# Kernel tuning notes

Measured on AMD Instinct MI355X. Metric: run time of the kernel, lower is better.

The kernel has to match this reference:

```python
import jax, jax.numpy as jnp
import numpy as np

N_WINDOWS = 4
WIN_H, WIN_W = 512, 512          # module 'size'
IMG_H, IMG_W = 1024, 1024        # 2x2 tiling of windows
N_MASKS = 32                     # n_windows * masks_per_window
MPW = N_MASKS // N_WINDOWS       # 8 masks per window (channel 0 of each block = background)
SLOT_DIM = 64
SIM_THRESH = 0.1                 # module 'similarity'


def setup_inputs() -> dict:
    key = jax.random.key(0)
    k1, k2 = jax.random.split(key)
    masks = jax.random.normal(k1, (1, N_MASKS, IMG_H, IMG_W), dtype=jnp.float32)
    slot_features = jax.random.normal(k2, (N_WINDOWS, MPW - 1, SLOT_DIM), dtype=jnp.float32)
    # static window layout, equivalent to keys ['w_0_0','w_512_0','w_0_512','w_512_512']
    pad_left = jnp.array([0, WIN_W, 0, WIN_W], dtype=jnp.int32)
    pad_top = jnp.array([0, 0, WIN_H, WIN_H], dtype=jnp.int32)
    return {"masks": masks, "slot_features": slot_features,
            "pad_left": pad_left, "pad_top": pad_top}


def _merge_windows(masks, slot_features, pl, pt):
    """pl, pt: python int lists (static metadata parsed from keys)."""
    B, C, H, W = masks.shape
    mpw = C // N_WINDOWS

    # --- to_one_hot: argmax over channel dim, one-hot back to [B,C,H,W] float ---
    ids = jnp.argmax(masks, axis=1)                                   # [B,H,W]
    m = jnp.moveaxis(jax.nn.one_hot(ids, C, dtype=masks.dtype), -1, 1)  # [B,C,H,W]

    ranges = [(i * mpw, (i + 1) * mpw) for i in range(N_WINDOWS)]

    # --- adjacency over window pads (static) ---
    adjacency = []
    for i in range(N_WINDOWS):
        for j in range(i + 1, N_WINDOWS):
            if pt[i] == pt[j] and abs(pl[i] - pl[j]) == WIN_W:
                adjacency.append((i, j, True) if pl[i] < pl[j] else (j, i, True))
            if pl[i] == pl[j] and abs(pt[i] - pt[j]) == WIN_H:
                adjacency.append((i, j, False) if pt[i] < pt[j] else (j, i, False))

    # --- per-channel edge-touch booleans (vectorized replacement of set building) ---
    edge_l = jnp.zeros((C,), bool)
    edge_r = jnp.zeros((C,), bool)
    edge_t = jnp.zeros((C,), bool)
    edge_b = jnp.zeros((C,), bool)
    for wi, (s, e) in enumerate(ranges):
        ys, ye = max(pt[wi], 0), min(pt[wi] + WIN_H, H)
        xs, xe = max(pl[wi], 0), min(pl[wi] + WIN_W, W)
        if ys >= ye or xs >= xe:
            continue
        win = m[0, s:e, ys:ye, xs:xe]                # [mpw, hh, ww]
        edge_l = edge_l.at[s:e].set(jnp.any(win[:, :, 0] == 1, axis=-1))
        edge_r = edge_r.at[s:e].set(jnp.any(win[:, :, -1] == 1, axis=-1))
        edge_t = edge_t.at[s:e].set(jnp.any(win[:, 0, :] == 1, axis=-1))
        edge_b = edge_b.at[s:e].set(jnp.any(win[:, -1, :] == 1, axis=-1))

    # --- static candidate pair list (background channels ci % mpw == 0 excluded) ---
    ci_l, cj_l, wi_l, wj_l, hz_l = [], [], [], [], []
    for wi, wj, horiz in adjacency:
        si, ei = ranges[wi]
        sj, ej = ranges[wj]
        for ci in range(si + 1, ei):
            for cj in range(sj + 1, ej):
                ci_l.append(ci); cj_l.append(cj)
                wi_l.append(wi); wj_l.append(wj); hz_l.append(horiz)
    P = len(ci_l)
    if P == 0:
        return m

    ci_a = jnp.array(ci_l, jnp.int32)
    cj_a = jnp.array(cj_l, jnp.int32)
    horiz = jnp.array(hz_l)

    # --- cosine similarities for all pairs at once ---
    sf_n = slot_features / (jnp.linalg.norm(slot_features, axis=-1, keepdims=True) + 1e-8)
    rel_i = np.array(ci_l) % mpw - 1
    rel_j = np.array(cj_l) % mpw - 1
    fi = sf_n[np.array(wi_l), rel_i]                 # [P, D]
    fj = sf_n[np.array(wj_l), rel_j]
    sims = jnp.sum(fi * fj, axis=-1)                 # [P]

    edge_ok = jnp.where(horiz, edge_r[ci_a] & edge_l[cj_a], edge_b[ci_a] & edge_t[cj_a])
    passing = edge_ok & (sims > SIM_THRESH)          # [P]

    # --- sequential dedup/merge scan (order-dependent, like the torch loop) ---
    def step(carry, xs):
        m, merged = carry
        ci, cj, ok = xs
        cond = ok & ~merged[ci] & ~merged[cj]
        keep = jnp.minimum(ci, cj)
        rem = jnp.maximum(ci, cj)
        rem_ch = jnp.take(m, rem, axis=1)            # [B,H,W]
        m = m.at[:, keep].add(jnp.where(cond, rem_ch, 0.0))
        m = m.at[:, rem].set(jnp.where(cond, jnp.zeros_like(rem_ch), rem_ch))
        merged = merged.at[rem].set(merged[rem] | cond)
        return (m, merged), None

    (m, _), _ = jax.lax.scan(step, (m, jnp.zeros((C,), bool)), (ci_a, cj_a, passing))
    return m


def reference(masks, slot_features, pad_left, pad_top):
    # pads encode the (static) window layout parsed from the string keys
    pl = [int(v) for v in np.asarray(pad_left)]
    pt = [int(v) for v in np.asarray(pad_top)]
    return _merge_windows(masks, slot_features, pl, pt)
```

## Files before the change

### kernel.cpp

```cpp
#include <hip/hip_runtime.h>

#define IMG_H 1024
#define IMG_W 1024
#define NPIX (IMG_H * IMG_W)
#define N_MASKS 32
#define N_WINDOWS 4
#define MPW 8
#define WIN_H 512
#define WIN_W 512
#define SIM_THRESH 0.1f
#define NBLK 1024

typedef float vf4 __attribute__((ext_vector_type(4)));

#define WS_EDGE  0
#define WS_IDS   (NBLK * 16)

__global__ __launch_bounds__(256) void k_argmax(const float* __restrict__ masks,
                                                const int* __restrict__ pl,
                                                const int* __restrict__ pt,
                                                uint4* __restrict__ edge_blocks,
                                                unsigned char* __restrict__ ids) {
    __shared__ int spl[4], spt[4];
    __shared__ unsigned sem[4];
    const int tid = threadIdx.x;
    if (tid < 4) { spl[tid] = pl[tid]; spt[tid] = pt[tid]; sem[tid] = 0u; }
    __syncthreads();

    const int idx = (blockIdx.x * 256 + tid) * 4;

    float bv0, bv1, bv2, bv3;
    int bc0 = 0, bc1 = 0, bc2 = 0, bc3 = 0;
    {
        const float4 v = *(const float4*)(masks + idx);
        bv0 = v.x; bv1 = v.y; bv2 = v.z; bv3 = v.w;
    }
#pragma unroll
    for (int c = 1; c < N_MASKS; c++) {
        const float4 v = *(const float4*)(masks + (size_t)c * NPIX + idx);
        if (v.x > bv0) { bv0 = v.x; bc0 = c; }
        if (v.y > bv1) { bv1 = v.y; bc1 = c; }
        if (v.z > bv2) { bv2 = v.z; bc2 = c; }
        if (v.w > bv3) { bv3 = v.w; bc3 = c; }
    }
    *(uchar4*)(ids + idx) = make_uchar4((unsigned char)bc0, (unsigned char)bc1,
                                        (unsigned char)bc2, (unsigned char)bc3);

    const int y = idx >> 10;
    const int x0 = idx & (IMG_W - 1);
    const int bcs[4] = {bc0, bc1, bc2, bc3};
#pragma unroll
    for (int wi = 0; wi < N_WINDOWS; wi++) {
        const int xs = max(spl[wi], 0), xe = min(spl[wi] + WIN_W, IMG_W);
        const int ys = max(spt[wi], 0), ye = min(spt[wi] + WIN_H, IMG_H);
        if (ys >= ye || xs >= xe) continue;
        if (y < ys || y >= ye) continue;
#pragma unroll
        for (int k = 0; k < 4; k++) {
            const int x = x0 + k;
            if (x < xs || x >= xe) continue;
            const int c = bcs[k];
            if ((c >> 3) != wi) continue;
            const unsigned bit = 1u << c;
            if (x == xs)     atomicOr(&sem[0], bit);
            if (x == xe - 1) atomicOr(&sem[1], bit);
            if (y == ys)     atomicOr(&sem[2], bit);
            if (y == ye - 1) atomicOr(&sem[3], bit);
        }
    }
    __syncthreads();
    if (tid == 0) edge_blocks[blockIdx.x] = make_uint4(sem[0], sem[1], sem[2], sem[3]);
}

__global__ __launch_bounds__(256) void k_merge_write(const unsigned char* __restrict__ ids,
                                                     const float* __restrict__ sf,
                                                     const int* __restrict__ pl,
                                                     const int* __restrict__ pt,
                                                     const uint4* __restrict__ edge_blocks,
                                                     float* __restrict__ out) {
    __shared__ float sfn[28 * 65];
    __shared__ unsigned step_word[512];
    __shared__ uint4 wred[4];
    __shared__ unsigned fedge[4];
    __shared__ int sP;
    __shared__ int loc[32];

    const int tid = threadIdx.x;
    const int lane = tid & 63;
    const int wave = tid >> 6;

    unsigned el = 0, er = 0, et = 0, eb = 0;
    for (int b = tid; b < NBLK; b += 256) {
        const uint4 w = edge_blocks[b];
        el |= w.x; er |= w.y; et |= w.z; eb |= w.w;
    }
#pragma unroll
    for (int off = 1; off < 64; off <<= 1) {
        el |= __shfl_xor(el, off);
        er |= __shfl_xor(er, off);
        et |= __shfl_xor(et, off);
        eb |= __shfl_xor(eb, off);
    }
    if (lane == 0) wred[wave] = make_uint4(el, er, et, eb);

#pragma unroll
    for (int i = 0; i < 7; i++) {
        const int r = wave + 4 * i;
        const float v = sf[r * 64 + lane];
        float s = v * v;
#pragma unroll
        for (int off = 1; off < 64; off <<= 1) s += __shfl_xor(s, off);
        sfn[r * 65 + lane] = v * (1.0f / (sqrtf(s) + 1e-8f));
    }
    __syncthreads();

    if (tid == 0) {
        unsigned fl = wred[0].x | wred[1].x | wred[2].x | wred[3].x;
        unsigned fr = wred[0].y | wred[1].y | wred[2].y | wred[3].y;
        unsigned ft = wred[0].z | wred[1].z | wred[2].z | wred[3].z;
        unsigned fb = wred[0].w | wred[1].w | wred[2].w | wred[3].w;
        fedge[0] = fl; fedge[1] = fr; fedge[2] = ft; fedge[3] = fb;

        int lpl[4], lpt[4];
        for (int i = 0; i < 4; i++) { lpl[i] = pl[i]; lpt[i] = pt[i]; }
        int aI[8], aJ[8], aH[8], na = 0;
        for (int i = 0; i < N_WINDOWS; i++)
            for (int j = i + 1; j < N_WINDOWS; j++) {
                if (lpt[i] == lpt[j] && abs(lpl[i] - lpl[j]) == WIN_W) {
                    if (lpl[i] < lpl[j]) { aI[na] = i; aJ[na] = j; }
                    else                 { aI[na] = j; aJ[na] = i; }
                    aH[na] = 1; na++;
                }
                if (lpl[i] == lpl[j] && abs(lpt[i] - lpt[j]) == WIN_H) {
                    if (lpt[i] < lpt[j]) { aI[na] = i; aJ[na] = j; }
                    else                 { aI[na] = j; aJ[na] = i; }
                    aH[na] = 0; na++;
                }
            }
        int P = 0;
        for (int a = 0; a < na; a++)
            for (int ci = aI[a] * MPW + 1; ci < (aI[a] + 1) * MPW; ci++)
                for (int cj = aJ[a] * MPW + 1; cj < (aJ[a] + 1) * MPW; cj++)
                    step_word[P++] = (unsigned)ci | ((unsigned)cj << 8)
                                   | ((unsigned)aH[a] << 16);
        sP = P;
    }
    __syncthreads();

    const int P = sP;
    {
        const unsigned ger = fedge[1], gel = fedge[0], geb = fedge[3], get = fedge[2];
        for (int p = tid; p < P; p += 256) {
            const unsigned w = step_word[p];
            const int ci = w & 255, cj = (w >> 8) & 255, hz = (w >> 16) & 1;
            const float* fi = &sfn[((ci >> 3) * (MPW - 1) + (ci & 7) - 1) * 65];
            const float* fj = &sfn[((cj >> 3) * (MPW - 1) + (cj & 7) - 1) * 65];
            float s = 0.f;
#pragma unroll
            for (int k = 0; k < 64; k++) s += fi[k] * fj[k];
            const bool eok = hz ? (((ger >> ci) & 1u) && ((gel >> cj) & 1u))
                                : (((geb >> ci) & 1u) && ((get >> cj) & 1u));
            if (eok && s > SIM_THRESH) step_word[p] = w | (1u << 17);
        }
    }
    __syncthreads();

    if (wave == 0) {
        unsigned merged = 0;
        int myloc = lane;
        for (int p = 0; p < P; p++) {
            const unsigned w = step_word[p];
            if (w >> 17) {
                const int ci = w & 255, cj = (w >> 8) & 255;
                if (!((merged >> ci) & 1u) && !((merged >> cj) & 1u)) {
                    const int keep = min(ci, cj), rem = max(ci, cj);
                    if (myloc == rem) myloc = keep;
                    merged |= 1u << rem;
                }
            }
        }
        if (lane < 32) loc[lane] = myloc;
    }
    __syncthreads();

    const int idx = (blockIdx.x * 256 + tid) * 4;
    const uchar4 id4 = *(const uchar4*)(ids + idx);
    const int r0 = loc[id4.x], r1 = loc[id4.y], r2 = loc[id4.z], r3 = loc[id4.w];
#pragma unroll
    for (int c = 0; c < N_MASKS; c++) {
        vf4 v;
        v.x = (r0 == c) ? 1.0f : 0.0f;
        v.y = (r1 == c) ? 1.0f : 0.0f;
        v.z = (r2 == c) ? 1.0f : 0.0f;
        v.w = (r3 == c) ? 1.0f : 0.0f;
        __builtin_nontemporal_store(v, (vf4*)(out + (size_t)c * NPIX + idx));
    }
}

extern "C" void kernel_launch(void* const* d_in, const int* in_sizes, int n_in,
                              void* d_out, int out_size, void* d_ws, size_t ws_size,
                              hipStream_t stream) {
    const float* masks = (const float*)d_in[0];
    const float* sf    = (const float*)d_in[1];
    const int*   pl    = (const int*)d_in[2];
    const int*   pt    = (const int*)d_in[3];
    float* out = (float*)d_out;

    char* ws = (char*)d_ws;
    uint4* edge_blocks = (uint4*)(ws + WS_EDGE);
    unsigned char* ids = (unsigned char*)(ws + WS_IDS);

    k_argmax<<<NBLK, 256, 0, stream>>>(masks, pl, pt, edge_blocks, ids);
    k_merge_write<<<NBLK, 256, 0, stream>>>(ids, sf, pl, pt, edge_blocks, out);
}
```

Before: 261.7 us.

## Process 16 pixels per thread with 256 blocks and nontemporal mask loads

Both kernels now give each thread 16 pixels (four float4 chunks) across 256 blocks instead of 4 pixels across 1024 blocks. This puts more independent loads in flight per thread and cuts per-block overhead, including the redundant per-block merge-table setup in the second kernel and the edge-block reduction size. Mask reads in the argmax kernel also switch to nontemporal loads. The cost is higher register pressure and fewer waves in flight, which could hurt latency hiding on a bandwidth-bound workload.

Result: faster. 255.5 us (-2.4%).

```diff
diff --git a/kernel.cpp b/kernel.cpp
--- a/kernel.cpp
+++ b/kernel.cpp
@@ -9,7 +9,9 @@
 #define WIN_H 512
 #define WIN_W 512
 #define SIM_THRESH 0.1f
-#define NBLK 1024
+
+#define NBLK 256
+#define PXB  4096
 
 typedef float vf4 __attribute__((ext_vector_type(4)));
 
@@ -27,45 +29,59 @@
     if (tid < 4) { spl[tid] = pl[tid]; spt[tid] = pt[tid]; sem[tid] = 0u; }
     __syncthreads();
 
-    const int idx = (blockIdx.x * 256 + tid) * 4;
-
-    float bv0, bv1, bv2, bv3;
-    int bc0 = 0, bc1 = 0, bc2 = 0, bc3 = 0;
-    {
-        const float4 v = *(const float4*)(masks + idx);
-        bv0 = v.x; bv1 = v.y; bv2 = v.z; bv3 = v.w;
+    const int wave = tid >> 6;
+    const int lane = tid & 63;
+    const int base = blockIdx.x * PXB + wave * 1024 + lane * 4;
+
+    float bv[16];
+    int   bc[16];
+#pragma unroll
+    for (int k = 0; k < 4; k++) {
+        const vf4 v = __builtin_nontemporal_load((const vf4*)(masks + base + k * 256));
+        bv[4*k+0] = v.x; bv[4*k+1] = v.y; bv[4*k+2] = v.z; bv[4*k+3] = v.w;
+        bc[4*k+0] = 0;   bc[4*k+1] = 0;   bc[4*k+2] = 0;   bc[4*k+3] = 0;
     }
 #pragma unroll
     for (int c = 1; c < N_MASKS; c++) {
-        const float4 v = *(const float4*)(masks + (size_t)c * NPIX + idx);
-        if (v.x > bv0) { bv0 = v.x; bc0 = c; }
-        if (v.y > bv1) { bv1 = v.y; bc1 = c; }
-        if (v.z > bv2) { bv2 = v.z; bc2 = c; }
-        if (v.w > bv3) { bv3 = v.w; bc3 = c; }
-    }
-    *(uchar4*)(ids + idx) = make_uchar4((unsigned char)bc0, (unsigned char)bc1,
-                                        (unsigned char)bc2, (unsigned char)bc3);
-
-    const int y = idx >> 10;
-    const int x0 = idx & (IMG_W - 1);
-    const int bcs[4] = {bc0, bc1, bc2, bc3};
-#pragma unroll
-    for (int wi = 0; wi < N_WINDOWS; wi++) {
-        const int xs = max(spl[wi], 0), xe = min(spl[wi] + WIN_W, IMG_W);
-        const int ys = max(spt[wi], 0), ye = min(spt[wi] + WIN_H, IMG_H);
-        if (ys >= ye || xs >= xe) continue;
-        if (y < ys || y >= ye) continue;
+        const float* mc = masks + (size_t)c * NPIX + base;
 #pragma unroll
         for (int k = 0; k < 4; k++) {
-            const int x = x0 + k;
-            if (x < xs || x >= xe) continue;
-            const int c = bcs[k];
-            if ((c >> 3) != wi) continue;
-            const unsigned bit = 1u << c;
-            if (x == xs)     atomicOr(&sem[0], bit);
-            if (x == xe - 1) atomicOr(&sem[1], bit);
-            if (y == ys)     atomicOr(&sem[2], bit);
-            if (y == ye - 1) atomicOr(&sem[3], bit);
+            const vf4 v = __builtin_nontemporal_load((const vf4*)(mc + k * 256));
+            if (v.x > bv[4*k+0]) { bv[4*k+0] = v.x; bc[4*k+0] = c; }
+            if (v.y > bv[4*k+1]) { bv[4*k+1] = v.y; bc[4*k+1] = c; }
+            if (v.z > bv[4*k+2]) { bv[4*k+2] = v.z; bc[4*k+2] = c; }
+            if (v.w > bv[4*k+3]) { bv[4*k+3] = v.w; bc[4*k+3] = c; }
+        }
+    }
+#pragma unroll
+    for (int k = 0; k < 4; k++)
+        *(uchar4*)(ids + base + k * 256) =
+            make_uchar4((unsigned char)bc[4*k+0], (unsigned char)bc[4*k+1],
+                        (unsigned char)bc[4*k+2], (unsigned char)bc[4*k+3]);
+
+#pragma unroll
+    for (int k = 0; k < 4; k++) {
+        const int px = base + k * 256;
+        const int y  = px >> 10;
+        const int x0 = px & (IMG_W - 1);
+#pragma unroll
+        for (int wi = 0; wi < N_WINDOWS; wi++) {
+            const int xs = max(spl[wi], 0), xe = min(spl[wi] + WIN_W, IMG_W);
+            const int ys = max(spt[wi], 0), ye = min(spt[wi] + WIN_H, IMG_H);
+            if (ys >= ye || xs >= xe) continue;
+            if (y < ys || y >= ye) continue;
+#pragma unroll
+            for (int j = 0; j < 4; j++) {
+                const int x = x0 + j;
+                if (x < xs || x >= xe) continue;
+                const int c = bc[4*k+j];
+                if ((c >> 3) != wi) continue;
+                const unsigned bit = 1u << c;
+                if (x == xs)     atomicOr(&sem[0], bit);
+                if (x == xe - 1) atomicOr(&sem[1], bit);
+                if (y == ys)     atomicOr(&sem[2], bit);
+                if (y == ye - 1) atomicOr(&sem[3], bit);
+            }
         }
     }
     __syncthreads();
@@ -183,17 +199,26 @@
     }
     __syncthreads();
 
-    const int idx = (blockIdx.x * 256 + tid) * 4;
-    const uchar4 id4 = *(const uchar4*)(ids + idx);
-    const int r0 = loc[id4.x], r1 = loc[id4.y], r2 = loc[id4.z], r3 = loc[id4.w];
+    const int base = blockIdx.x * PXB + wave * 1024 + lane * 4;
+    int r[16];
+#pragma unroll
+    for (int k = 0; k < 4; k++) {
+        const uchar4 id4 = *(const uchar4*)(ids + base + k * 256);
+        r[4*k+0] = loc[id4.x]; r[4*k+1] = loc[id4.y];
+        r[4*k+2] = loc[id4.z]; r[4*k+3] = loc[id4.w];
+    }
 #pragma unroll
     for (int c = 0; c < N_MASKS; c++) {
-        vf4 v;
-        v.x = (r0 == c) ? 1.0f : 0.0f;
-        v.y = (r1 == c) ? 1.0f : 0.0f;
-        v.z = (r2 == c) ? 1.0f : 0.0f;
-        v.w = (r3 == c) ? 1.0f : 0.0f;
-        __builtin_nontemporal_store(v, (vf4*)(out + (size_t)c * NPIX + idx));
+        float* oc = out + (size_t)c * NPIX + base;
+#pragma unroll
+        for (int k = 0; k < 4; k++) {
+            vf4 v;
+            v.x = (r[4*k+0] == c) ? 1.0f : 0.0f;
+            v.y = (r[4*k+1] == c) ? 1.0f : 0.0f;
+            v.z = (r[4*k+2] == c) ? 1.0f : 0.0f;
+            v.w = (r[4*k+3] == c) ? 1.0f : 0.0f;
+            __builtin_nontemporal_store(v, (vf4*)(oc + k * 256));
+        }
     }
 }
 
```
